# Optimization experiments

Measured on AMD Instinct MI355X. Metric: run time of the kernel, lower is better.

## Reference

```python
import jax, jax.numpy as jnp
import numpy as np
from jax import lax

FILTER_DIM = 11  # FIR taps
BATCH = 128
N = 262144  # samples per frame
CHANNELS = 1
STRIDES = 1


def setup_inputs() -> dict:
    key = jax.random.key(0)
    kx, kp = jax.random.split(key)
    X = jax.random.normal(kx, (BATCH, N, 2), dtype=jnp.float32)
    # learned FIR filter: (filter_dim, 2, channels) -> [:,0,:]=real taps, [:,1,:]=imag taps
    phi = jax.random.normal(kp, (FILTER_DIM, 2, CHANNELS), dtype=jnp.float32)
    return {"X": X, "phi": phi}


def _conv1d(x, w):
    # x: (B, N, 1), w: (K, 1, 1); TF-style SAME cross-correlation, channels_last
    return lax.conv_general_dilated(
        x, w, window_strides=(STRIDES,), padding="SAME",
        dimension_numbers=("NWC", "WIO", "NWC"))


def reference(X, phi):
    # X: (B, N, 2) complex as [real, imag]; phi: (K, 2, 1)
    X_real = X[:, :, 0:1]            # (B, N, 1)
    X_img = X[:, :, 1:2]             # (B, N, 1)
    phi_real = phi[:, 0, :][:, None, :]  # (K, 1, 1)
    phi_img = phi[:, 1, :][:, None, :]   # (K, 1, 1)
    # complex convolution: (Xr + i Xi) * (pr + i pi)
    real = _conv1d(X_real, phi_real) - _conv1d(X_img, phi_img)  # (B, N, 1)
    img = _conv1d(X_real, phi_img) + _conv1d(X_img, phi_real)   # (B, N, 1)
    return jnp.concatenate([real, img], axis=2)  # (B, N, 2)
```

## Files before the change

### kernel.cpp

```cpp
#include <hip/hip_runtime.h>


constexpr int N_SAMP  = 262144;
constexpr int BATCH   = 128;
constexpr int TAPS    = 11;
constexpr int HALO    = 5;
constexpr int BLOCK   = 256;
constexpr int VEC     = 4;
constexpr int TILE    = BLOCK * VEC;
constexpr int SMEM_N  = TILE + 2 * HALO;

__global__ __launch_bounds__(BLOCK)
void fir_complex_kernel(const float2* __restrict__ X,
                        const float*  __restrict__ phi,
                        float2*       __restrict__ out)
{
    __shared__ float2 s[SMEM_N];

    const int tile_idx   = blockIdx.x;
    const int b          = blockIdx.y;
    const int t          = threadIdx.x;
    const int tile_start = tile_idx * TILE;
    const long long row  = (long long)b * N_SAMP;

    float pr[TAPS], pi[TAPS];
#pragma unroll
    for (int k = 0; k < TAPS; ++k) {
        pr[k] = phi[2 * k + 0];
        pi[k] = phi[2 * k + 1];
    }

    const int g0 = tile_start - HALO;
#pragma unroll
    for (int r = 0; r < (SMEM_N + BLOCK - 1) / BLOCK; ++r) {
        const int i = r * BLOCK + t;
        if (i < SMEM_N) {
            const int n = g0 + i;
            float2 v = make_float2(0.0f, 0.0f);
            if ((unsigned)n < (unsigned)N_SAMP) v = X[row + n];
            s[i] = v;
        }
    }
    __syncthreads();

#pragma unroll
    for (int j = 0; j < VEC; ++j) {
        const int l = t + j * BLOCK;
        float re = 0.0f, im = 0.0f;
#pragma unroll
        for (int k = 0; k < TAPS; ++k) {
            const float2 v = s[l + k];
            re = fmaf(v.x, pr[k], re);
            re = fmaf(-v.y, pi[k], re);
            im = fmaf(v.x, pi[k], im);
            im = fmaf(v.y, pr[k], im);
        }
        out[row + tile_start + l] = make_float2(re, im);
    }
}

extern "C" void kernel_launch(void* const* d_in, const int* in_sizes, int n_in,
                              void* d_out, int out_size, void* d_ws, size_t ws_size,
                              hipStream_t stream)
{
    const float2* X   = (const float2*)d_in[0];
    const float*  phi = (const float*)d_in[1];
    float2*       out = (float2*)d_out;

    dim3 grid(N_SAMP / TILE, BATCH);
    fir_complex_kernel<<<grid, BLOCK, 0, stream>>>(X, phi, out);
}
```

Before: 423.1 us.

## Split shared memory into planar real/imag arrays and compute two outputs per thread

The tile is loaded with float4 global reads and deinterleaved into separate real and imaginary shared arrays. Each thread then computes two adjacent outputs from a 14-sample register window and writes them with a single float4 store. The tile doubles to 2048 samples per block, halving the grid. This is meant to cut shared-memory loads per output and widen global accesses. The cost is more registers and fewer blocks. The kernel is likely memory bound already, so the benefit may be small.

```diff
diff --git a/kernel.cpp b/kernel.cpp
--- a/kernel.cpp
+++ b/kernel.cpp
@@ -4,24 +4,24 @@
 constexpr int N_SAMP  = 262144;
 constexpr int BATCH   = 128;
 constexpr int TAPS    = 11;
-constexpr int HALO    = 5;
 constexpr int BLOCK   = 256;
-constexpr int VEC     = 4;
-constexpr int TILE    = BLOCK * VEC;
-constexpr int SMEM_N  = TILE + 2 * HALO;
+constexpr int PAIRS   = 4;
+constexpr int TILE    = BLOCK * PAIRS * 2;
+constexpr int PAD     = 6;
+constexpr int N_SLOTS = TILE / 2 + PAD;
+constexpr int SMEM_N  = 2 * N_SLOTS;
 
 __global__ __launch_bounds__(BLOCK)
 void fir_complex_kernel(const float2* __restrict__ X,
                         const float*  __restrict__ phi,
                         float2*       __restrict__ out)
 {
-    __shared__ float2 s[SMEM_N];
+    __shared__ __align__(16) float s_re[SMEM_N];
+    __shared__ __align__(16) float s_im[SMEM_N];
 
-    const int tile_idx   = blockIdx.x;
-    const int b          = blockIdx.y;
     const int t          = threadIdx.x;
-    const int tile_start = tile_idx * TILE;
-    const long long row  = (long long)b * N_SAMP;
+    const int tile_start = blockIdx.x * TILE;
+    const long long row  = (long long)blockIdx.y * N_SAMP;
 
     float pr[TAPS], pi[TAPS];
 #pragma unroll
@@ -30,32 +30,54 @@
         pi[k] = phi[2 * k + 1];
     }
 
-    const int g0 = tile_start - HALO;
+    const float4* __restrict__ X4 = reinterpret_cast<const float4*>(X);
+    const int g0 = tile_start - PAD;
 #pragma unroll
-    for (int r = 0; r < (SMEM_N + BLOCK - 1) / BLOCK; ++r) {
-        const int i = r * BLOCK + t;
-        if (i < SMEM_N) {
-            const int n = g0 + i;
-            float2 v = make_float2(0.0f, 0.0f);
-            if ((unsigned)n < (unsigned)N_SAMP) v = X[row + n];
-            s[i] = v;
+    for (int r = 0; r < (N_SLOTS + BLOCK - 1) / BLOCK; ++r) {
+        const int i4 = r * BLOCK + t;
+        if (i4 < N_SLOTS) {
+            const int g = g0 + 2 * i4;
+            float4 v = make_float4(0.f, 0.f, 0.f, 0.f);
+            if ((unsigned)g < (unsigned)N_SAMP)
+                v = X4[(row + g) >> 1];
+            *reinterpret_cast<float2*>(&s_re[2 * i4]) = make_float2(v.x, v.z);
+            *reinterpret_cast<float2*>(&s_im[2 * i4]) = make_float2(v.y, v.w);
         }
     }
     __syncthreads();
 
+    float4* __restrict__ out4 = reinterpret_cast<float4*>(out);
 #pragma unroll
-    for (int j = 0; j < VEC; ++j) {
-        const int l = t + j * BLOCK;
-        float re = 0.0f, im = 0.0f;
+    for (int j = 0; j < PAIRS; ++j) {
+        const int l = 2 * t + j * (2 * BLOCK);
+
+        float wre[14], wim[14];
+#pragma unroll
+        for (int q = 0; q < 7; ++q) {
+            const float2 a = *reinterpret_cast<const float2*>(&s_re[l + 2 * q]);
+            const float2 b = *reinterpret_cast<const float2*>(&s_im[l + 2 * q]);
+            wre[2 * q]     = a.x;
+            wre[2 * q + 1] = a.y;
+            wim[2 * q]     = b.x;
+            wim[2 * q + 1] = b.y;
+        }
+
+        float r0 = 0.f, i0 = 0.f, r1 = 0.f, i1 = 0.f;
 #pragma unroll
         for (int k = 0; k < TAPS; ++k) {
-            const float2 v = s[l + k];
-            re = fmaf(v.x, pr[k], re);
-            re = fmaf(-v.y, pi[k], re);
-            im = fmaf(v.x, pi[k], im);
-            im = fmaf(v.y, pr[k], im);
+            const float xr0 = wre[k + 1], xi0 = wim[k + 1];
+            const float xr1 = wre[k + 2], xi1 = wim[k + 2];
+            r0 = fmaf(xr0,  pr[k], r0);
+            r0 = fmaf(-xi0, pi[k], r0);
+            i0 = fmaf(xr0,  pi[k], i0);
+            i0 = fmaf(xi0,  pr[k], i0);
+            r1 = fmaf(xr1,  pr[k], r1);
+            r1 = fmaf(-xi1, pi[k], r1);
+            i1 = fmaf(xr1,  pi[k], i1);
+            i1 = fmaf(xi1,  pr[k], i1);
         }
-        out[row + tile_start + l] = make_float2(re, im);
+
+        out4[(row + tile_start + l) >> 1] = make_float4(r0, i0, r1, i1);
     }
 }
 
```

After: 431.6 us. +2.0%, slower.
